# Optimization experiments

Measured on AMD Instinct MI355X. Metric: run time of the kernel, lower is better.

## Reference

```python
import jax, jax.numpy as jnp
import numpy as np

ROUTING_ITERS = 3

def squash(t, axis=-1):
    norm = jnp.linalg.norm(t, axis=axis, keepdims=True)
    scale = norm ** 2 / (1 + norm ** 2)
    return scale * t / (norm + 1e-08)

def setup_inputs() -> dict:
    key = jax.random.key(0)
    k1, k2 = jax.random.split(key)
    B, R, C, Din, Dout = 64, 4608, 32, 16, 16
    x = jax.random.normal(k1, (B, R, Din), dtype=jnp.float32)
    route_weights = jax.random.normal(k2, (R, C, Din, Dout), dtype=jnp.float32)
    return {"x": x, "route_weights": route_weights}

def reference(x, route_weights):
    # x: [B, R, Din], route_weights: [R, C, Din, Dout]
    B, R, _ = x.shape
    C = route_weights.shape[1]
    # u_hat: [B, R, C, Dout]  (prediction vectors)
    u_hat = jnp.einsum('bri,rcio->brco', x, route_weights)
    b_ij = jnp.zeros((B, R, C, 1), dtype=u_hat.dtype)
    v_j = None
    for _ in range(ROUTING_ITERS):
        c_ij = jax.nn.softmax(b_ij, axis=2)                    # coupling coeffs over capsules
        s_j = jnp.sum(c_ij * u_hat, axis=1, keepdims=True)     # [B, 1, C, Dout]
        v_j = squash(s_j, axis=-1)                             # [B, 1, C, Dout]
        b_ij = b_ij + jnp.sum(u_hat * v_j, axis=-1, keepdims=True)
    return v_j[:, 0]                                           # [B, C, Dout]
```

## Files before the change

### kernel.cpp

```cpp
#include <hip/hip_runtime.h>
#include <math.h>


#define B_    64
#define R_    4608
#define C_    32
#define RB    36
#define NBLK  (R_ / RB)
#define SELEM 32768

typedef _Float16 half8  __attribute__((ext_vector_type(8)));
typedef _Float16 half2v __attribute__((ext_vector_type(2)));
typedef float    f32x16 __attribute__((ext_vector_type(16)));

__device__ __forceinline__ void gload_lds16(const void* g, void* l) {
    __builtin_amdgcn_global_load_lds(
        (const __attribute__((address_space(1))) void*)g,
        (__attribute__((address_space(3))) void*)l, 16, 0, 0);
}

__global__ __launch_bounds__(512)
void caps_prep(const float* __restrict__ x, _Float16* __restrict__ xa)
{
    __shared__ _Float16 tl[8][64][16];
    const int t  = threadIdx.x;
    const int r0 = blockIdx.x * 8;

    {
        const int b = t >> 3, j8 = t & 7;
        const float4* xs = (const float4*)(x + ((size_t)b * R_ + r0 + j8) * 16);
        const float4 A = xs[0], Bv = xs[1], Cv = xs[2], Dv = xs[3];
        half8 lo, hi;
        lo[0]=(_Float16)A.x;  lo[1]=(_Float16)A.y;  lo[2]=(_Float16)A.z;  lo[3]=(_Float16)A.w;
        lo[4]=(_Float16)Bv.x; lo[5]=(_Float16)Bv.y; lo[6]=(_Float16)Bv.z; lo[7]=(_Float16)Bv.w;
        hi[0]=(_Float16)Cv.x; hi[1]=(_Float16)Cv.y; hi[2]=(_Float16)Cv.z; hi[3]=(_Float16)Cv.w;
        hi[4]=(_Float16)Dv.x; hi[5]=(_Float16)Dv.y; hi[6]=(_Float16)Dv.z; hi[7]=(_Float16)Dv.w;
        *(half8*)&tl[j8][b][0] = lo;
        *(half8*)&tl[j8][b][8] = hi;
    }
    __syncthreads();
    {
        const int rl = t >> 6, q = t & 63;
        _Float16* dst = xa + (size_t)(r0 + rl) * 1024 + q * 16;
        *(half8*)dst       = *(const half8*)&tl[rl][q][0];
        *(half8*)(dst + 8) = *(const half8*)&tl[rl][q][8];
    }
}

template<bool FIRST>
__global__ __launch_bounds__(1024, 4)
void caps_mfma(const _Float16* __restrict__ xa, const float* __restrict__ Wg,
               _Float16* __restrict__ wp, const float* __restrict__ vsumT,
               float* __restrict__ sdst)
{
    __shared__ _Float16 xalds[RB * 512];
    __shared__ float tc_lds[2][32][33];

    const int D     = blockIdx.x;
    const int xcd   = D & 7;
    const int slot  = D >> 3;
    const int chunk = (slot >> 1) * 8 + xcd;
    const int bh    = slot & 1;

    const int tid  = threadIdx.x;
    const int lane = tid & 63;
    const int wv   = tid >> 6;
    const int h    = lane >> 5;
    const int l31  = lane & 31;
    const int r0   = chunk * RB;
    const int bg   = bh * 32 + l31;

    {
        const int slx = (lane << 4) ^ (((lane >> 3) & 7) << 4);
        for (int t = wv; t < RB; t += 16) {
            const char* src = (const char*)xa + (size_t)(r0 + t) * 2048 + bh * 1024 + slx;
            gload_lds16(src, (char*)xalds + t * 1024);
        }
    }

    f32x16 sacc, zf;
#pragma unroll
    for (int k = 0; k < 16; ++k) { sacc[k] = 0.f; zf[k] = 0.f; }

    half2v vh[8];
    if (!FIRST) {
#pragma unroll
        for (int e = 0; e < 16; ++e) {
            const int g = wv * 32 + (e & 3) + 8 * (e >> 2) + 4 * h;
            vh[e >> 1][e & 1] = (_Float16)vsumT[(size_t)g * 64 + bg];
        }
    }

    asm volatile("s_waitcnt vmcnt(0)" ::: "memory");
    __syncthreads();

    const int avoff = ((l31 << 5) + (h << 4)) ^ (((l31 >> 2) & 7) << 4);

    const int c_ = 2 * wv + (l31 >> 4);
    const int o_ = l31 & 15;
#define WGATHER(dst, r)                                                           \
    do {                                                                          \
        const float* ws_ = Wg + (((size_t)(r) * 32 + c_) * 16 + 8 * h) * 16 + o_; \
        _Pragma("unroll")                                                         \
        for (int e_ = 0; e_ < 8; ++e_) dst[e_] = (_Float16)ws_[e_ * 16];          \
    } while (0)

    const size_t wstride = 16 * 64 * 8;

    if (FIRST) {
        half8 bc;
        WGATHER(bc, r0);
#pragma unroll 1
        for (int t = 0; t < RB; ++t) {
            const half8 av = *(const half8*)((const char*)xalds + t * 1024 + avoff);
            sacc = __builtin_amdgcn_mfma_f32_32x32x16_f16(bc, av, sacc, 0, 0, 0);
            if (bh == 0)
                *(half8*)(wp + (((size_t)(r0 + t) * 16 + wv) * 64 + lane) * 8) = bc;
            if (t + 1 < RB) WGATHER(bc, r0 + t + 1);
        }
    } else {
        const _Float16* wpb = wp + ((size_t)wv * 64 + lane) * 8;
        half8 bc0 = *(const half8*)(wpb + (size_t)(r0    ) * wstride);
        half8 bc1 = *(const half8*)(wpb + (size_t)(r0 + 1) * wstride);

#pragma unroll 1
        for (int t = 0; t < RB; t += 2) {
            const half8 av0 = *(const half8*)((const char*)xalds + (t    ) * 1024 + avoff);
            const half8 av1 = *(const half8*)((const char*)xalds + (t + 1) * 1024 + avoff);

            const f32x16 u0 = __builtin_amdgcn_mfma_f32_32x32x16_f16(bc0, av0, zf, 0, 0, 0);
            const f32x16 u1 = __builtin_amdgcn_mfma_f32_32x32x16_f16(bc1, av1, zf, 0, 0, 0);

            const int tn = (t + 2 < RB) ? (t + 2) : t;
            bc0 = *(const half8*)(wpb + (size_t)(r0 + tn    ) * wstride);
            bc1 = *(const half8*)(wpb + (size_t)(r0 + tn + 1) * wstride);

            {
                float a0 = 0.f, a1 = 0.f, b0 = 0.f, b1 = 0.f;
#pragma unroll
                for (int e2 = 0; e2 < 4; ++e2) {
                    a0 += u0[2 * e2]         * (float)vh[e2][0];
                    a0 += u0[2 * e2 + 1]     * (float)vh[e2][1];
                    a1 += u0[8 + 2 * e2]     * (float)vh[4 + e2][0];
                    a1 += u0[8 + 2 * e2 + 1] * (float)vh[4 + e2][1];
                    b0 += u1[2 * e2]         * (float)vh[e2][0];
                    b0 += u1[2 * e2 + 1]     * (float)vh[e2][1];
                    b1 += u1[8 + 2 * e2]     * (float)vh[4 + e2][0];
                    b1 += u1[8 + 2 * e2 + 1] * (float)vh[4 + e2][1];
                }
                a0 += __shfl_xor(a0, 32);
                a1 += __shfl_xor(a1, 32);
                b0 += __shfl_xor(b0, 32);
                b1 += __shfl_xor(b1, 32);
                if (h == 0) {
                    tc_lds[0][2 * wv    ][l31] = a0;
                    tc_lds[0][2 * wv + 1][l31] = a1;
                    tc_lds[1][2 * wv    ][l31] = b0;
                    tc_lds[1][2 * wv + 1][l31] = b1;
                }
            }
            __syncthreads();

            {
                const int rr   = tid >> 9;
                const int tid5 = tid & 511;
                const int a_   = tid5 & 15;
                const int b2   = tid5 >> 4;
                const float tA = tc_lds[rr][2 * a_][b2];
                const float tB = tc_lds[rr][2 * a_ + 1][b2];
                float m = fmaxf(tA, tB);
                m = fmaxf(m, __shfl_xor(m, 1));
                m = fmaxf(m, __shfl_xor(m, 2));
                m = fmaxf(m, __shfl_xor(m, 4));
                m = fmaxf(m, __shfl_xor(m, 8));
                const float eA = __expf(tA - m);
                const float eB = __expf(tB - m);
                float zs = eA + eB;
                zs += __shfl_xor(zs, 1);
                zs += __shfl_xor(zs, 2);
                zs += __shfl_xor(zs, 4);
                zs += __shfl_xor(zs, 8);
                const float inv = 1.0f / zs;
                tc_lds[rr][2 * a_][b2]     = eA * inv;
                tc_lds[rr][2 * a_ + 1][b2] = eB * inv;
            }
            __syncthreads();

            {
                const float c00 = tc_lds[0][2 * wv    ][l31];
                const float c01 = tc_lds[0][2 * wv + 1][l31];
                const float c10 = tc_lds[1][2 * wv    ][l31];
                const float c11 = tc_lds[1][2 * wv + 1][l31];
#pragma unroll
                for (int e = 0; e < 8; ++e)
                    sacc[e] += c00 * u0[e] + c10 * u1[e];
#pragma unroll
                for (int e = 8; e < 16; ++e)
                    sacc[e] += c01 * u0[e] + c11 * u1[e];
            }
        }
    }
#undef WGATHER

    const float scale = FIRST ? 0.03125f : 1.0f;
    float* sp = sdst + ((size_t)chunk << 15);
#pragma unroll
    for (int e = 0; e < 16; ++e) {
        const int g = wv * 32 + (e & 3) + 8 * (e >> 2) + 4 * h;
        sp[(size_t)g * 64 + bg] = sacc[e] * scale;
    }
}

__global__ __launch_bounds__(256)
void caps_reduce1(const float* __restrict__ sp, float* __restrict__ s2)
{
    const int e  = blockIdx.x * 256 + threadIdx.x;
    const int pg = blockIdx.y;
    const float* p0 = sp + (size_t)pg * 16 * SELEM + e;
    float a = 0.0f;
#pragma unroll 8
    for (int p = 0; p < 16; ++p) a += p0[(size_t)p * SELEM];
    s2[pg * SELEM + e] = a;
}

__global__ __launch_bounds__(64)
void caps_reduce2T(const float* __restrict__ src, float* __restrict__ vsumT,
                   float* __restrict__ out, int mode)
{
    const int c = blockIdx.x;
    const int b = threadIdx.x;
    float a[16];
#pragma unroll
    for (int o = 0; o < 16; ++o) a[o] = 0.0f;
    for (int p = 0; p < 8; ++p)
#pragma unroll
        for (int o = 0; o < 16; ++o)
            a[o] += src[(size_t)p * SELEM + c * 1024 + o * 64 + b];
    float sq = 0.0f;
#pragma unroll
    for (int o = 0; o < 16; ++o) sq += a[o] * a[o];
    const float n  = sqrtf(sq);
    const float sc = sq / (1.0f + sq) / (n + 1e-8f);
    if (mode == 2) {
#pragma unroll
        for (int o = 0; o < 16; ++o)
            out[(size_t)b * 512 + c * 16 + o] = a[o] * sc;
    } else if (mode == 0) {
#pragma unroll
        for (int o = 0; o < 16; ++o)
            vsumT[c * 1024 + o * 64 + b] = a[o] * sc;
    } else {
#pragma unroll
        for (int o = 0; o < 16; ++o)
            vsumT[c * 1024 + o * 64 + b] += a[o] * sc;
    }
}

__global__ __launch_bounds__(256)
void caps_reduce2(const float* __restrict__ src, int P,
                  float* __restrict__ vsum, float* __restrict__ out, int mode)
{
    const int e = blockIdx.x * 256 + threadIdx.x;
    float a = 0.0f;
    for (int p = 0; p < P; ++p) a += src[(size_t)p * SELEM + e];
    float sq = a * a;
#pragma unroll
    for (int off = 8; off >= 1; off >>= 1) sq += __shfl_xor(sq, off);
    const float n = sqrtf(sq);
    const float v = a * (sq / (1.0f + sq) / (n + 1e-8f));
    if (mode == 0)      vsum[e] = v;
    else if (mode == 1) vsum[e] += v;
    else                out[e] = v;
}

template<bool FIRST>
__global__ __launch_bounds__(1024, 4)
void caps_pass_f32(const float* __restrict__ x, const float* __restrict__ W,
                   const float* __restrict__ vsumg, float* __restrict__ sdst)
{
    __shared__ float wlds[2][8192];
    const int tid = threadIdx.x, lane = tid & 63;
    const int c = tid & 31, dh = (tid >> 5) & 1, w = tid >> 6;
    const int r0 = blockIdx.x * RB, b0 = w << 2;
    const int key = (c & 7) << 4;
    const int cb  = (c << 10) + (dh << 5);

    float sacc[4][8];
#pragma unroll
    for (int q = 0; q < 4; ++q)
#pragma unroll
        for (int k = 0; k < 8; ++k) sacc[q][k] = 0.0f;

    float vreg[4][8];
    if (!FIRST) {
#pragma unroll
        for (int q = 0; q < 4; ++q) {
            const float4* vp = (const float4*)(vsumg + ((((b0+q) << 5) + c) << 4) + (dh << 3));
            float4 a = vp[0], bq = vp[1];
            vreg[q][0]=a.x; vreg[q][1]=a.y; vreg[q][2]=a.z; vreg[q][3]=a.w;
            vreg[q][4]=bq.x; vreg[q][5]=bq.y; vreg[q][6]=bq.z; vreg[q][7]=bq.w;
        }
    }

    const int Dloc0 = (w << 11);
    const int lx0 = (lane << 4) ^ ((((w << 1))     & 7) << 4);
    const int lx1 = (lane << 4) ^ ((((w << 1) | 1) & 7) << 4);
    const int wu = __builtin_amdgcn_readfirstlane(w);
    const float* xw = x + (size_t)((wu << 2) * R_ + r0) * 16;

#define STAGE(buf, r)                                                              \
    do {                                                                           \
        const char* wr_ = (const char*)W + ((size_t)(r) << 15);                    \
        gload_lds16(wr_ + Dloc0        + lx0, (char*)wlds[buf] + Dloc0);           \
        gload_lds16(wr_ + Dloc0 + 1024 + lx1, (char*)wlds[buf] + Dloc0 + 1024);    \
    } while (0)

    STAGE(0, r0);
#pragma unroll 1
    for (int t = 0; t < RB; ++t) {
        const int cur = t & 1;
        if (t + 1 < RB) { STAGE(cur ^ 1, r0 + t + 1); asm volatile("s_waitcnt vmcnt(2)" ::: "memory"); }
        else            { asm volatile("s_waitcnt vmcnt(0)" ::: "memory"); }
        __builtin_amdgcn_s_barrier();
        __builtin_amdgcn_sched_barrier(0);

        const char* lb = (const char*)wlds[cur];
        float u[4][8];
#pragma unroll
        for (int q = 0; q < 4; ++q)
#pragma unroll
            for (int k = 0; k < 8; ++k) u[q][k] = 0.0f;

#pragma unroll
        for (int i = 0; i < 16; ++i) {
            const int A = (cb + (i << 6)) ^ key;
            float4 w0 = *(const float4*)(lb + A);
            float4 w1 = *(const float4*)(lb + (A ^ 16));
            float wv[8] = {w0.x, w0.y, w0.z, w0.w, w1.x, w1.y, w1.z, w1.w};
#pragma unroll
            for (int q = 0; q < 4; ++q) {
                const float xv = xw[(size_t)q * (R_ * 16) + t * 16 + i];
#pragma unroll
                for (int k = 0; k < 8; ++k) u[q][k] = fmaf(xv, wv[k], u[q][k]);
            }
        }

#pragma unroll
        for (int q = 0; q < 4; ++q) {
            float cij;
            if (FIRST) cij = 0.03125f;
            else {
                float th = 0.0f;
#pragma unroll
                for (int k = 0; k < 8; ++k) th = fmaf(u[q][k], vreg[q][k], th);
                th += __shfl_xor(th, 32);
                float m = th;
#pragma unroll
                for (int off = 16; off >= 1; off >>= 1) m = fmaxf(m, __shfl_xor(m, off));
                const float e = __expf(th - m);
                float ssum = e;
#pragma unroll
                for (int off = 16; off >= 1; off >>= 1) ssum += __shfl_xor(ssum, off);
                cij = e / ssum;
            }
#pragma unroll
            for (int k = 0; k < 8; ++k) sacc[q][k] = fmaf(cij, u[q][k], sacc[q][k]);
        }
        __builtin_amdgcn_s_barrier();
    }
#undef STAGE

#pragma unroll
    for (int q = 0; q < 4; ++q) {
        float* sp = sdst + ((((b0+q) << 5) + c) << 4) + (dh << 3);
#pragma unroll
        for (int k = 0; k < 8; ++k) atomicAdd(sp + k, sacc[q][k]);
    }
}

extern "C" void kernel_launch(void* const* d_in, const int* in_sizes, int n_in,
                              void* d_out, int out_size, void* d_ws, size_t ws_size,
                              hipStream_t stream)
{
    const float* x = (const float*)d_in[0];
    const float* W = (const float*)d_in[1];
    float* out = (float*)d_out;

    const size_t WPB = (size_t)R_ * 16 * 64 * 8 * sizeof(_Float16);
    const size_t XAB = (size_t)R_ * 64 * 16 * sizeof(_Float16);
    const size_t SPB = (size_t)NBLK * SELEM * sizeof(float);
    const size_t S2B = (size_t)8 * SELEM * sizeof(float);
    const size_t VSB = (size_t)SELEM * sizeof(float);
    char* wsc = (char*)d_ws;

    if (ws_size >= WPB + XAB + SPB + S2B + VSB) {
        _Float16* wp  = (_Float16*)wsc;
        _Float16* xa  = (_Float16*)(wsc + WPB);
        float* s_part = (float*)(wsc + WPB + XAB);
        float* s2     = (float*)(wsc + WPB + XAB + SPB);
        float* vsumT  = (float*)(wsc + WPB + XAB + SPB + S2B);

        caps_prep<<<576, 512, 0, stream>>>(x, xa);

        caps_mfma<true ><<<256, 1024, 0, stream>>>(xa, W, wp, nullptr, s_part);
        caps_reduce1<<<dim3(128, 8), 256, 0, stream>>>(s_part, s2);
        caps_reduce2T<<<32, 64, 0, stream>>>(s2, vsumT, nullptr, 0);

        caps_mfma<false><<<256, 1024, 0, stream>>>(xa, W, wp, vsumT, s_part);
        caps_reduce1<<<dim3(128, 8), 256, 0, stream>>>(s_part, s2);
        caps_reduce2T<<<32, 64, 0, stream>>>(s2, vsumT, nullptr, 1);

        caps_mfma<false><<<256, 1024, 0, stream>>>(xa, W, wp, vsumT, s_part);
        caps_reduce1<<<dim3(128, 8), 256, 0, stream>>>(s_part, s2);
        caps_reduce2T<<<32, 64, 0, stream>>>(s2, vsumT, out, 2);
    } else {
        float* s    = (float*)wsc;
        float* vsum = s + SELEM;

        hipMemsetAsync(s, 0, VSB, stream);
        caps_pass_f32<true><<<NBLK, 1024, 0, stream>>>(x, W, nullptr, s);
        caps_reduce2<<<128, 256, 0, stream>>>(s, 1, vsum, nullptr, 0);

        hipMemsetAsync(s, 0, VSB, stream);
        caps_pass_f32<false><<<NBLK, 1024, 0, stream>>>(x, W, vsum, s);
        caps_reduce2<<<128, 256, 0, stream>>>(s, 1, vsum, nullptr, 1);

        hipMemsetAsync(s, 0, VSB, stream);
        caps_pass_f32<false><<<NBLK, 1024, 0, stream>>>(x, W, vsum, s);
        caps_reduce2<<<128, 256, 0, stream>>>(s, 1, nullptr, out, 2);
    }
}
```

Baseline: 139.6 us.

## Fuse x fp16 conversion into MFMA kernel and merge two-stage reduction

Removes the separate prep kernel that converted x to a transposed fp16 buffer. Each MFMA block now loads the fp32 x tile directly, converts it, and writes it swizzled into LDS. The two-stage partial-sum reduction is also collapsed into one kernel that sums all partials and applies squash via LDS. The fp32 fallback path is dropped. This saves launches and an intermediate buffer, but each MFMA pass now re-reads fp32 x with strided loads, and the single reduce kernel uses only 32 blocks.

New measurement: 138.8 us. About the same (-0.6%).

```diff
diff --git a/kernel.cpp b/kernel.cpp
--- a/kernel.cpp
+++ b/kernel.cpp
@@ -10,46 +10,13 @@
 #define SELEM 32768
 
 typedef _Float16 half8  __attribute__((ext_vector_type(8)));
+typedef _Float16 half4v __attribute__((ext_vector_type(4)));
 typedef _Float16 half2v __attribute__((ext_vector_type(2)));
 typedef float    f32x16 __attribute__((ext_vector_type(16)));
 
-__device__ __forceinline__ void gload_lds16(const void* g, void* l) {
-    __builtin_amdgcn_global_load_lds(
-        (const __attribute__((address_space(1))) void*)g,
-        (__attribute__((address_space(3))) void*)l, 16, 0, 0);
-}
-
-__global__ __launch_bounds__(512)
-void caps_prep(const float* __restrict__ x, _Float16* __restrict__ xa)
-{
-    __shared__ _Float16 tl[8][64][16];
-    const int t  = threadIdx.x;
-    const int r0 = blockIdx.x * 8;
-
-    {
-        const int b = t >> 3, j8 = t & 7;
-        const float4* xs = (const float4*)(x + ((size_t)b * R_ + r0 + j8) * 16);
-        const float4 A = xs[0], Bv = xs[1], Cv = xs[2], Dv = xs[3];
-        half8 lo, hi;
-        lo[0]=(_Float16)A.x;  lo[1]=(_Float16)A.y;  lo[2]=(_Float16)A.z;  lo[3]=(_Float16)A.w;
-        lo[4]=(_Float16)Bv.x; lo[5]=(_Float16)Bv.y; lo[6]=(_Float16)Bv.z; lo[7]=(_Float16)Bv.w;
-        hi[0]=(_Float16)Cv.x; hi[1]=(_Float16)Cv.y; hi[2]=(_Float16)Cv.z; hi[3]=(_Float16)Cv.w;
-        hi[4]=(_Float16)Dv.x; hi[5]=(_Float16)Dv.y; hi[6]=(_Float16)Dv.z; hi[7]=(_Float16)Dv.w;
-        *(half8*)&tl[j8][b][0] = lo;
-        *(half8*)&tl[j8][b][8] = hi;
-    }
-    __syncthreads();
-    {
-        const int rl = t >> 6, q = t & 63;
-        _Float16* dst = xa + (size_t)(r0 + rl) * 1024 + q * 16;
-        *(half8*)dst       = *(const half8*)&tl[rl][q][0];
-        *(half8*)(dst + 8) = *(const half8*)&tl[rl][q][8];
-    }
-}
-
 template<bool FIRST>
 __global__ __launch_bounds__(1024, 4)
-void caps_mfma(const _Float16* __restrict__ xa, const float* __restrict__ Wg,
+void caps_mfma(const float* __restrict__ x, const float* __restrict__ Wg,
                _Float16* __restrict__ wp, const float* __restrict__ vsumT,
                float* __restrict__ sdst)
 {
@@ -71,10 +38,20 @@
     const int bg   = bh * 32 + l31;
 
     {
-        const int slx = (lane << 4) ^ (((lane >> 3) & 7) << 4);
-        for (int t = wv; t < RB; t += 16) {
-            const char* src = (const char*)xa + (size_t)(r0 + t) * 2048 + bh * 1024 + slx;
-            gload_lds16(src, (char*)xalds + t * 1024);
+        const float* xbase = x + (size_t)(bh * 32) * (R_ * 16);
+        for (int i = tid; i < RB * 32 * 4; i += 1024) {
+            const int b_   = i / (RB * 4);
+            const int rem  = i - b_ * (RB * 4);
+            const int rloc = rem >> 2;
+            const int part = rem & 3;
+            const float4 v = *(const float4*)(xbase + (size_t)b_ * (R_ * 16)
+                                              + (size_t)(r0 + rloc) * 16 + part * 4);
+            half4v f;
+            f[0] = (_Float16)v.x; f[1] = (_Float16)v.y;
+            f[2] = (_Float16)v.z; f[3] = (_Float16)v.w;
+            const int P = rloc * 1024 + b_ * 32 + part * 8;
+            const int A = P ^ (((P >> 7) & 7) << 4);
+            *(half4v*)((char*)xalds + A) = f;
         }
     }
 
@@ -91,7 +68,6 @@
         }
     }
 
-    asm volatile("s_waitcnt vmcnt(0)" ::: "memory");
     __syncthreads();
 
     const int avoff = ((l31 << 5) + (h << 4)) ^ (((l31 >> 2) & 7) << 4);
@@ -211,171 +187,30 @@
     }
 }
 
-__global__ __launch_bounds__(256)
-void caps_reduce1(const float* __restrict__ sp, float* __restrict__ s2)
+__global__ __launch_bounds__(1024)
+void caps_reduce(const float* __restrict__ sp, float* __restrict__ vsumT,
+                 float* __restrict__ out, int mode)
 {
-    const int e  = blockIdx.x * 256 + threadIdx.x;
-    const int pg = blockIdx.y;
-    const float* p0 = sp + (size_t)pg * 16 * SELEM + e;
-    float a = 0.0f;
+    __shared__ float sq_lds[16][64];
+    const int c   = blockIdx.x;
+    const int tid = threadIdx.x;
+
+    float a = 0.f;
 #pragma unroll 8
-    for (int p = 0; p < 16; ++p) a += p0[(size_t)p * SELEM];
-    s2[pg * SELEM + e] = a;
-}
-
-__global__ __launch_bounds__(64)
-void caps_reduce2T(const float* __restrict__ src, float* __restrict__ vsumT,
-                   float* __restrict__ out, int mode)
-{
-    const int c = blockIdx.x;
-    const int b = threadIdx.x;
-    float a[16];
-#pragma unroll
-    for (int o = 0; o < 16; ++o) a[o] = 0.0f;
-    for (int p = 0; p < 8; ++p)
-#pragma unroll
-        for (int o = 0; o < 16; ++o)
-            a[o] += src[(size_t)p * SELEM + c * 1024 + o * 64 + b];
-    float sq = 0.0f;
-#pragma unroll
-    for (int o = 0; o < 16; ++o) sq += a[o] * a[o];
-    const float n  = sqrtf(sq);
-    const float sc = sq / (1.0f + sq) / (n + 1e-8f);
-    if (mode == 2) {
-#pragma unroll
-        for (int o = 0; o < 16; ++o)
-            out[(size_t)b * 512 + c * 16 + o] = a[o] * sc;
-    } else if (mode == 0) {
-#pragma unroll
-        for (int o = 0; o < 16; ++o)
-            vsumT[c * 1024 + o * 64 + b] = a[o] * sc;
-    } else {
-#pragma unroll
-        for (int o = 0; o < 16; ++o)
-            vsumT[c * 1024 + o * 64 + b] += a[o] * sc;
-    }
-}
-
-__global__ __launch_bounds__(256)
-void caps_reduce2(const float* __restrict__ src, int P,
-                  float* __restrict__ vsum, float* __restrict__ out, int mode)
-{
-    const int e = blockIdx.x * 256 + threadIdx.x;
-    float a = 0.0f;
-    for (int p = 0; p < P; ++p) a += src[(size_t)p * SELEM + e];
-    float sq = a * a;
-#pragma unroll
-    for (int off = 8; off >= 1; off >>= 1) sq += __shfl_xor(sq, off);
+    for (int p = 0; p < NBLK; ++p)
+        a += sp[(size_t)p * SELEM + c * 1024 + tid];
+
+    sq_lds[tid >> 6][tid & 63] = a * a;
+    __syncthreads();
+    float sq = 0.f;
+#pragma unroll
+    for (int o = 0; o < 16; ++o) sq += sq_lds[o][tid & 63];
     const float n = sqrtf(sq);
     const float v = a * (sq / (1.0f + sq) / (n + 1e-8f));
-    if (mode == 0)      vsum[e] = v;
-    else if (mode == 1) vsum[e] += v;
-    else                out[e] = v;
-}
-
-template<bool FIRST>
-__global__ __launch_bounds__(1024, 4)
-void caps_pass_f32(const float* __restrict__ x, const float* __restrict__ W,
-                   const float* __restrict__ vsumg, float* __restrict__ sdst)
-{
-    __shared__ float wlds[2][8192];
-    const int tid = threadIdx.x, lane = tid & 63;
-    const int c = tid & 31, dh = (tid >> 5) & 1, w = tid >> 6;
-    const int r0 = blockIdx.x * RB, b0 = w << 2;
-    const int key = (c & 7) << 4;
-    const int cb  = (c << 10) + (dh << 5);
-
-    float sacc[4][8];
-#pragma unroll
-    for (int q = 0; q < 4; ++q)
-#pragma unroll
-        for (int k = 0; k < 8; ++k) sacc[q][k] = 0.0f;
-
-    float vreg[4][8];
-    if (!FIRST) {
-#pragma unroll
-        for (int q = 0; q < 4; ++q) {
-            const float4* vp = (const float4*)(vsumg + ((((b0+q) << 5) + c) << 4) + (dh << 3));
-            float4 a = vp[0], bq = vp[1];
-            vreg[q][0]=a.x; vreg[q][1]=a.y; vreg[q][2]=a.z; vreg[q][3]=a.w;
-            vreg[q][4]=bq.x; vreg[q][5]=bq.y; vreg[q][6]=bq.z; vreg[q][7]=bq.w;
-        }
-    }
-
-    const int Dloc0 = (w << 11);
-    const int lx0 = (lane << 4) ^ ((((w << 1))     & 7) << 4);
-    const int lx1 = (lane << 4) ^ ((((w << 1) | 1) & 7) << 4);
-    const int wu = __builtin_amdgcn_readfirstlane(w);
-    const float* xw = x + (size_t)((wu << 2) * R_ + r0) * 16;
-
-#define STAGE(buf, r)                                                              \
-    do {                                                                           \
-        const char* wr_ = (const char*)W + ((size_t)(r) << 15);                    \
-        gload_lds16(wr_ + Dloc0        + lx0, (char*)wlds[buf] + Dloc0);           \
-        gload_lds16(wr_ + Dloc0 + 1024 + lx1, (char*)wlds[buf] + Dloc0 + 1024);    \
-    } while (0)
-
-    STAGE(0, r0);
-#pragma unroll 1
-    for (int t = 0; t < RB; ++t) {
-        const int cur = t & 1;
-        if (t + 1 < RB) { STAGE(cur ^ 1, r0 + t + 1); asm volatile("s_waitcnt vmcnt(2)" ::: "memory"); }
-        else            { asm volatile("s_waitcnt vmcnt(0)" ::: "memory"); }
-        __builtin_amdgcn_s_barrier();
-        __builtin_amdgcn_sched_barrier(0);
-
-        const char* lb = (const char*)wlds[cur];
-        float u[4][8];
-#pragma unroll
-        for (int q = 0; q < 4; ++q)
-#pragma unroll
-            for (int k = 0; k < 8; ++k) u[q][k] = 0.0f;
-
-#pragma unroll
-        for (int i = 0; i < 16; ++i) {
-            const int A = (cb + (i << 6)) ^ key;
-            float4 w0 = *(const float4*)(lb + A);
-            float4 w1 = *(const float4*)(lb + (A ^ 16));
-            float wv[8] = {w0.x, w0.y, w0.z, w0.w, w1.x, w1.y, w1.z, w1.w};
-#pragma unroll
-            for (int q = 0; q < 4; ++q) {
-                const float xv = xw[(size_t)q * (R_ * 16) + t * 16 + i];
-#pragma unroll
-                for (int k = 0; k < 8; ++k) u[q][k] = fmaf(xv, wv[k], u[q][k]);
-            }
-        }
-
-#pragma unroll
-        for (int q = 0; q < 4; ++q) {
-            float cij;
-            if (FIRST) cij = 0.03125f;
-            else {
-                float th = 0.0f;
-#pragma unroll
-                for (int k = 0; k < 8; ++k) th = fmaf(u[q][k], vreg[q][k], th);
-                th += __shfl_xor(th, 32);
-                float m = th;
-#pragma unroll
-                for (int off = 16; off >= 1; off >>= 1) m = fmaxf(m, __shfl_xor(m, off));
-                const float e = __expf(th - m);
-                float ssum = e;
-#pragma unroll
-                for (int off = 16; off >= 1; off >>= 1) ssum += __shfl_xor(ssum, off);
-                cij = e / ssum;
-            }
-#pragma unroll
-            for (int k = 0; k < 8; ++k) sacc[q][k] = fmaf(cij, u[q][k], sacc[q][k]);
-        }
-        __builtin_amdgcn_s_barrier();
-    }
-#undef STAGE
-
-#pragma unroll
-    for (int q = 0; q < 4; ++q) {
-        float* sp = sdst + ((((b0+q) << 5) + c) << 4) + (dh << 3);
-#pragma unroll
-        for (int k = 0; k < 8; ++k) atomicAdd(sp + k, sacc[q][k]);
-    }
+
+    if (mode == 0)      vsumT[c * 1024 + tid] = v;
+    else if (mode == 1) vsumT[c * 1024 + tid] += v;
+    else                out[(size_t)(tid & 63) * 512 + c * 16 + (tid >> 6)] = v;
 }
 
 extern "C" void kernel_launch(void* const* d_in, const int* in_sizes, int n_in,
@@ -387,46 +222,21 @@
     float* out = (float*)d_out;
 
     const size_t WPB = (size_t)R_ * 16 * 64 * 8 * sizeof(_Float16);
-    const size_t XAB = (size_t)R_ * 64 * 16 * sizeof(_Float16);
     const size_t SPB = (size_t)NBLK * SELEM * sizeof(float);
-    const size_t S2B = (size_t)8 * SELEM * sizeof(float);
     const size_t VSB = (size_t)SELEM * sizeof(float);
     char* wsc = (char*)d_ws;
-
-    if (ws_size >= WPB + XAB + SPB + S2B + VSB) {
-        _Float16* wp  = (_Float16*)wsc;
-        _Float16* xa  = (_Float16*)(wsc + WPB);
-        float* s_part = (float*)(wsc + WPB + XAB);
-        float* s2     = (float*)(wsc + WPB + XAB + SPB);
-        float* vsumT  = (float*)(wsc + WPB + XAB + SPB + S2B);
-
-        caps_prep<<<576, 512, 0, stream>>>(x, xa);
-
-        caps_mfma<true ><<<256, 1024, 0, stream>>>(xa, W, wp, nullptr, s_part);
-        caps_reduce1<<<dim3(128, 8), 256, 0, stream>>>(s_part, s2);
-        caps_reduce2T<<<32, 64, 0, stream>>>(s2, vsumT, nullptr, 0);
-
-        caps_mfma<false><<<256, 1024, 0, stream>>>(xa, W, wp, vsumT, s_part);
-        caps_reduce1<<<dim3(128, 8), 256, 0, stream>>>(s_part, s2);
-        caps_reduce2T<<<32, 64, 0, stream>>>(s2, vsumT, nullptr, 1);
-
-        caps_mfma<false><<<256, 1024, 0, stream>>>(xa, W, wp, vsumT, s_part);
-        caps_reduce1<<<dim3(128, 8), 256, 0, stream>>>(s_part, s2);
-        caps_reduce2T<<<32, 64, 0, stream>>>(s2, vsumT, out, 2);
-    } else {
-        float* s    = (float*)wsc;
-        float* vsum = s + SELEM;
-
-        hipMemsetAsync(s, 0, VSB, stream);
-        caps_pass_f32<true><<<NBLK, 1024, 0, stream>>>(x, W, nullptr, s);
-        caps_reduce2<<<128, 256, 0, stream>>>(s, 1, vsum, nullptr, 0);
-
-        hipMemsetAsync(s, 0, VSB, stream);
-        caps_pass_f32<false><<<NBLK, 1024, 0, stream>>>(x, W, vsum, s);
-        caps_reduce2<<<128, 256, 0, stream>>>(s, 1, vsum, nullptr, 1);
-
-        hipMemsetAsync(s, 0, VSB, stream);
-        caps_pass_f32<false><<<NBLK, 1024, 0, stream>>>(x, W, vsum, s);
-        caps_reduce2<<<128, 256, 0, stream>>>(s, 1, nullptr, out, 2);
-    }
+    if (ws_size < WPB + SPB + VSB) return;
+
+    _Float16* wp  = (_Float16*)wsc;
+    float* s_part = (float*)(wsc + WPB);
+    float* vsumT  = (float*)(wsc + WPB + SPB);
+
+    caps_mfma<true ><<<256, 1024, 0, stream>>>(x, W, wp, nullptr, s_part);
+    caps_reduce<<<32, 1024, 0, stream>>>(s_part, vsumT, nullptr, 0);
+
+    caps_mfma<false><<<256, 1024, 0, stream>>>(x, W, wp, vsumT, s_part);
+    caps_reduce<<<32, 1024, 0, stream>>>(s_part, vsumT, nullptr, 1);
+
+    caps_mfma<false><<<256, 1024, 0, stream>>>(x, W, wp, vsumT, s_part);
+    caps_reduce<<<32, 1024, 0, stream>>>(s_part, vsumT, out, 2);
 }
```
